# Optimization experiments

Measured on AMD Instinct MI355X. Metric: run time of the kernel, lower is better.

The kernel has to match this reference:

```python
import jax, jax.numpy as jnp
import numpy as np


def setup_inputs() -> dict:
    key = jax.random.key(0)
    kq, kk, kwq, kwk, kwv = jax.random.split(key, 5)
    B, T, C, H = 16, 2048, 1024, 64
    q = jax.random.normal(kq, (B, T, C), dtype=jnp.float32)
    k = jax.random.normal(kk, (B, T, C), dtype=jnp.float32)
    s = 1.0 / np.sqrt(C)
    Wq = jax.random.normal(kwq, (C, H), dtype=jnp.float32) * s
    Wk = jax.random.normal(kwk, (C, H), dtype=jnp.float32) * s
    Wv = jax.random.normal(kwv, (C, H), dtype=jnp.float32) * s
    return {"q": q, "k": k, "Wq": Wq, "Wk": Wk, "Wv": Wv}


def reference(q, k, Wq, Wk, Wv):
    # q, k: (B, T, C); projections are bias-free C -> head_size H
    Q = q @ Wq            # (B, T, H)
    K = k @ Wk            # (B, T, H)
    V = k @ Wv            # (B, T, H)
    T = q.shape[1]
    # NOTE: original scales by input dim C (q.shape[-1]), not head_size
    scale = q.shape[-1] ** (-0.5)
    wei = jnp.einsum('bth,bsh->bts', Q, K) * scale   # (B, T, T)
    causal = jnp.tril(jnp.ones((T, T), dtype=bool))
    wei = jnp.where(causal, wei, -jnp.inf)
    wei = jax.nn.softmax(wei, axis=-1)
    # dropout rate is 0.0 -> identity at inference
    out = jnp.einsum('bts,bsh->bth', wei, V)         # (B, T, H)
    return out
```

## Files before the change

kernel.cpp:

```cpp
#include <hip/hip_runtime.h>
#include <hip/hip_bf16.h>

typedef __bf16 bf16;
typedef __bf16 bf16x4 __attribute__((ext_vector_type(4)));
typedef __bf16 bf16x8 __attribute__((ext_vector_type(8)));
typedef float f32x4 __attribute__((ext_vector_type(4)));

#define MFMA_16x16x32(A, B, C) __builtin_amdgcn_mfma_f32_16x16x32_bf16(A, B, C, 0, 0, 0)

static_assert(sizeof(bf16x8) == 16, "bf16x8 must be 16B");

__global__ __launch_bounds__(256) void wtrans_kernel(
    const float* __restrict__ Wq, const float* __restrict__ Wk,
    const float* __restrict__ Wv, bf16* __restrict__ Wt)
{
  int idx = blockIdx.x * 256 + threadIdx.x;
  int p = idx >> 16;
  int rem = idx & 65535;
  int h = rem >> 10;
  int c = rem & 1023;
  const float* W = (p == 0) ? Wq : (p == 1) ? Wk : Wv;
  Wt[idx] = (bf16)W[c * 64 + h];
}

__global__ __launch_bounds__(1024, 4) void proj_kernel(
    const float* __restrict__ qin, const float* __restrict__ kin,
    const bf16* __restrict__ Wt,
    bf16* __restrict__ Qb, bf16* __restrict__ Kb, bf16* __restrict__ Vtb)
{
  extern __shared__ __align__(16) bf16 lds[];
  const int tid = threadIdx.x;
  const int lane = tid & 63;
  const int w = tid >> 6;
  const int g = lane >> 4;
  const int r = lane & 15;
  const int rl = lane >> 2;
  const int l4 = lane & 3;

  bf16* const stageW = lds + 65536 + w * 640;

  const int bid = blockIdx.x;
  const bool isQ = (bid < 128);
  const int fbid = isQ ? bid : bid - 128;
  const int strip = fbid * 16 + w;
  const float* A = isQ ? qin : kin;
  const float* ap = A + (size_t)strip * 16 * 1024;

  f32x4 acc0[4], acc1[4];
  #pragma unroll
  for (int cf = 0; cf < 4; cf++) {
    acc0[cf] = (f32x4){0.f, 0.f, 0.f, 0.f};
    acc1[cf] = (f32x4){0.f, 0.f, 0.f, 0.f};
  }

  auto afrag = [&](int c) -> bf16x8 {
    const float* rowp = ap + (size_t)rl * 1024 + c * 32 + l4 * 4;
    float4 a0 = *(const float4*)(rowp);
    float4 a1 = *(const float4*)(rowp + 16);
    bf16x4 w0 = (bf16x4){(bf16)a0.x, (bf16)a0.y, (bf16)a0.z, (bf16)a0.w};
    bf16x4 w1 = (bf16x4){(bf16)a1.x, (bf16)a1.y, (bf16)a1.z, (bf16)a1.w};
    *(bf16x4*)&stageW[rl * 40 + l4 * 4] = w0;
    *(bf16x4*)&stageW[rl * 40 + 16 + l4 * 4] = w1;
    return *(const bf16x8*)&stageW[r * 40 + g * 8];
  };

  if (isQ) {
    #pragma unroll
    for (int i = 0; i < 8; ++i) {
      int cid = i * 1024 + tid;
      int row = cid >> 7, ch = cid & 127;
      int pch = ch ^ (row & 7);
      *(bf16x8*)&lds[row * 1024 + pch * 8] =
          *(const bf16x8*)(Wt + (size_t)row * 1024 + ch * 8);
    }
    __syncthreads();

    #pragma unroll 2
    for (int c = 0; c < 32; ++c) {
      bf16x8 af = afrag(c);
      #pragma unroll
      for (int cf = 0; cf < 4; cf++) {
        int rw = cf * 16 + r;
        int pch = (4 * c + g) ^ (rw & 7);
        bf16x8 bfr = *(const bf16x8*)&lds[rw * 1024 + pch * 8];
        acc0[cf] = MFMA_16x16x32(af, bfr, acc0[cf]);
      }
    }

    #pragma unroll
    for (int cf = 0; cf < 4; cf++)
      #pragma unroll
      for (int jj = 0; jj < 4; jj++) {
        int rg = strip * 16 + g * 4 + jj;
        Qb[(size_t)rg * 64 + cf * 16 + r] = (bf16)acc0[cf][jj];
      }
  } else {
    for (int p = 0; p < 4; ++p) {
      __syncthreads();
      #pragma unroll
      for (int i = 0; i < 2; ++i) {
        int cid = i * 1024 + tid;
        int row = cid >> 5, ch = cid & 31;
        int pch = ch ^ (row & 7);
        *(bf16x8*)&lds[row * 256 + pch * 8] =
            *(const bf16x8*)(Wt + 65536 + (size_t)row * 1024 + p * 256 + ch * 8);
        *(bf16x8*)&lds[16384 + row * 256 + pch * 8] =
            *(const bf16x8*)(Wt + 2 * 65536 + (size_t)row * 1024 + p * 256 + ch * 8);
      }
      __syncthreads();

      #pragma unroll 2
      for (int cl = 0; cl < 8; ++cl) {
        bf16x8 af = afrag(p * 8 + cl);
        #pragma unroll
        for (int cf = 0; cf < 4; cf++) {
          int rw = cf * 16 + r;
          int pch = (4 * cl + g) ^ (rw & 7);
          bf16x8 b0 = *(const bf16x8*)&lds[rw * 256 + pch * 8];
          acc0[cf] = MFMA_16x16x32(af, b0, acc0[cf]);
          bf16x8 b1 = *(const bf16x8*)&lds[16384 + rw * 256 + pch * 8];
          acc1[cf] = MFMA_16x16x32(af, b1, acc1[cf]);
        }
      }
    }

    #pragma unroll
    for (int cf = 0; cf < 4; cf++)
      #pragma unroll
      for (int jj = 0; jj < 4; jj++) {
        int rg = strip * 16 + g * 4 + jj;
        Kb[(size_t)rg * 64 + cf * 16 + r] = (bf16)acc0[cf][jj];
      }
    int bb = (strip * 16) >> 11;
    int t0 = (strip * 16 + g * 4) & 2047;
    #pragma unroll
    for (int cf = 0; cf < 4; cf++) {
      bf16x4 v = (bf16x4){(bf16)acc1[cf][0], (bf16)acc1[cf][1],
                          (bf16)acc1[cf][2], (bf16)acc1[cf][3]};
      *(bf16x4*)&Vtb[((size_t)(bb * 64 + cf * 16 + r)) * 2048 + t0] = v;
    }
  }
}

__global__ __launch_bounds__(256) void attn_kernel(
    const bf16* __restrict__ Qb, const bf16* __restrict__ Kb,
    const bf16* __restrict__ Vtb, float* __restrict__ out)
{
  const int qt = (int)(gridDim.x - 1 - blockIdx.x);
  const int b = blockIdx.y;
  const int tid = threadIdx.x;
  const int lane = tid & 63;
  const int w = tid >> 6;
  const int g = lane >> 4;
  const int r = lane & 15;

  __shared__ __align__(16) bf16 Ks[64][80];
  __shared__ __align__(16) bf16 Vs[64][80];
  __shared__ __align__(16) bf16 Ps[4][16][80];

  const int q0 = qt * 64 + w * 16;
  const bf16* qp = Qb + (size_t)(b * 2048 + q0 + r) * 64 + g * 8;
  const bf16x8 qf0 = *(const bf16x8*)qp;
  const bf16x8 qf1 = *(const bf16x8*)(qp + 32);

  f32x4 acc_o[4];
  #pragma unroll
  for (int hf = 0; hf < 4; hf++) acc_o[hf] = (f32x4){0.f, 0.f, 0.f, 0.f};
  float m_r[4] = {-1e30f, -1e30f, -1e30f, -1e30f};
  float l_r[4] = {0.f, 0.f, 0.f, 0.f};
  const float scale = 0.03125f;

  const int sh = tid >> 2;
  const int sc = (tid & 3) * 16;

  for (int kv = 0; kv <= qt; kv++) {
    {
      const bf16* kp = Kb + (size_t)(b * 2048 + kv * 64 + sh) * 64 + sc;
      *(bf16x8*)&Ks[sh][sc]     = *(const bf16x8*)kp;
      *(bf16x8*)&Ks[sh][sc + 8] = *(const bf16x8*)(kp + 8);
      const bf16* vp = Vtb + (size_t)(b * 64 + sh) * 2048 + kv * 64 + sc;
      *(bf16x8*)&Vs[sh][sc]     = *(const bf16x8*)vp;
      *(bf16x8*)&Vs[sh][sc + 8] = *(const bf16x8*)(vp + 8);
    }
    __syncthreads();

    f32x4 s[4];
    #pragma unroll
    for (int cf = 0; cf < 4; cf++) {
      bf16x8 kf0 = *(const bf16x8*)&Ks[cf * 16 + r][g * 8];
      bf16x8 kf1 = *(const bf16x8*)&Ks[cf * 16 + r][32 + g * 8];
      f32x4 t = (f32x4){0.f, 0.f, 0.f, 0.f};
      t = MFMA_16x16x32(qf0, kf0, t);
      t = MFMA_16x16x32(qf1, kf1, t);
      s[cf] = t;
    }

    const bool diag = (kv == qt);
    float pm[4] = {-1e30f, -1e30f, -1e30f, -1e30f};
    #pragma unroll
    for (int cf = 0; cf < 4; cf++) {
      #pragma unroll
      for (int j = 0; j < 4; j++) {
        float v = s[cf][j] * scale;
        if (diag && (cf * 16 + r) > (w * 16 + g * 4 + j)) v = -1e30f;
        s[cf][j] = v;
        pm[j] = fmaxf(pm[j], v);
      }
    }
    #pragma unroll
    for (int j = 0; j < 4; j++) {
      #pragma unroll
      for (int msk = 1; msk < 16; msk <<= 1)
        pm[j] = fmaxf(pm[j], __shfl_xor(pm[j], msk, 64));
    }
    float corr[4];
    #pragma unroll
    for (int j = 0; j < 4; j++) {
      float mn = fmaxf(m_r[j], pm[j]);
      corr[j] = __expf(m_r[j] - mn);
      m_r[j] = mn;
    }
    float rs[4] = {0.f, 0.f, 0.f, 0.f};
    #pragma unroll
    for (int cf = 0; cf < 4; cf++) {
      #pragma unroll
      for (int j = 0; j < 4; j++) {
        float pv = __expf(s[cf][j] - m_r[j]);
        s[cf][j] = pv;
        rs[j] += pv;
      }
    }
    #pragma unroll
    for (int j = 0; j < 4; j++) {
      #pragma unroll
      for (int msk = 1; msk < 16; msk <<= 1)
        rs[j] += __shfl_xor(rs[j], msk, 64);
      l_r[j] = l_r[j] * corr[j] + rs[j];
    }
    #pragma unroll
    for (int hf = 0; hf < 4; hf++)
      #pragma unroll
      for (int j = 0; j < 4; j++)
        acc_o[hf][j] *= corr[j];

    #pragma unroll
    for (int cf = 0; cf < 4; cf++)
      #pragma unroll
      for (int j = 0; j < 4; j++)
        Ps[w][g * 4 + j][cf * 16 + r] = (bf16)s[cf][j];

    __syncthreads();

    #pragma unroll
    for (int ss = 0; ss < 2; ss++) {
      bf16x8 pf = *(const bf16x8*)&Ps[w][r][ss * 32 + g * 8];
      #pragma unroll
      for (int hf = 0; hf < 4; hf++) {
        bf16x8 vf = *(const bf16x8*)&Vs[hf * 16 + r][ss * 32 + g * 8];
        acc_o[hf] = MFMA_16x16x32(pf, vf, acc_o[hf]);
      }
    }
    __syncthreads();
  }

  float inv[4];
  #pragma unroll
  for (int j = 0; j < 4; j++) inv[j] = 1.0f / l_r[j];
  const size_t ob = (size_t)(b * 2048 + q0) * 64;
  #pragma unroll
  for (int hf = 0; hf < 4; hf++)
    #pragma unroll
    for (int j = 0; j < 4; j++)
      out[ob + (size_t)(g * 4 + j) * 64 + hf * 16 + r] = acc_o[hf][j] * inv[j];
}

extern "C" void kernel_launch(void* const* d_in, const int* in_sizes, int n_in,
                              void* d_out, int out_size, void* d_ws, size_t ws_size,
                              hipStream_t stream)
{
  const float* q  = (const float*)d_in[0];
  const float* k  = (const float*)d_in[1];
  const float* Wq = (const float*)d_in[2];
  const float* Wk = (const float*)d_in[3];
  const float* Wv = (const float*)d_in[4];
  float* out = (float*)d_out;

  char* ws = (char*)d_ws;
  bf16* Qb  = (bf16*)(ws);
  bf16* Kb  = (bf16*)(ws + (4u << 20));
  bf16* Vtb = (bf16*)(ws + (8u << 20));
  bf16* Wt  = (bf16*)(ws + (12u << 20));

  hipLaunchKernelGGL(wtrans_kernel, dim3(768), dim3(256), 0, stream,
                     Wq, Wk, Wv, Wt);
  hipLaunchKernelGGL(proj_kernel, dim3(256), dim3(1024), 151552, stream,
                     q, k, Wt, Qb, Kb, Vtb);
  hipLaunchKernelGGL(attn_kernel, dim3(32, 16), dim3(256), 0, stream,
                     Qb, Kb, Vtb, out);
}
```

Baseline: 125.9 us.

## Restructure projection kernel with batched A-loads, padded LDS, and smaller blocks

The projection kernel now runs 512 blocks of 512 threads (8 waves) instead of 256 blocks of 1024. Each wave loads a full 16x256 slab of activations with 16 coalesced float4 loads per lane before converting to bf16 into a padded LDS tile, replacing the per-MFMA gather-and-stage path. The Q and K/V paths share one four-phase loop over K with padded (stride-280) weight tiles instead of XOR swizzling. A __syncthreads between the P write and the PV MFMA in attention is also removed, relying on each wave only reading its own Ps slice, though other waves' Vs reads may still be constrained.

```diff
diff --git a/kernel.cpp b/kernel.cpp
--- a/kernel.cpp
+++ b/kernel.cpp
@@ -23,7 +23,7 @@
   Wt[idx] = (bf16)W[c * 64 + h];
 }
 
-__global__ __launch_bounds__(1024, 4) void proj_kernel(
+__global__ __launch_bounds__(512, 2) void proj_kernel(
     const float* __restrict__ qin, const float* __restrict__ kin,
     const bf16* __restrict__ Wt,
     bf16* __restrict__ Qb, bf16* __restrict__ Kb, bf16* __restrict__ Vtb)
@@ -34,17 +34,16 @@
   const int w = tid >> 6;
   const int g = lane >> 4;
   const int r = lane & 15;
-  const int rl = lane >> 2;
-  const int l4 = lane & 3;
-
-  bf16* const stageW = lds + 65536 + w * 640;
 
   const int bid = blockIdx.x;
-  const bool isQ = (bid < 128);
-  const int fbid = isQ ? bid : bid - 128;
-  const int strip = fbid * 16 + w;
+  const bool isQ = (bid < 256);
+  const int strip = (isQ ? bid : bid - 256) * 8 + w;
   const float* A = isQ ? qin : kin;
-  const float* ap = A + (size_t)strip * 16 * 1024;
+  const float* ap = A + (size_t)strip * 16 * 1024 + lane * 4;
+
+  bf16* const B0 = lds;
+  bf16* const B1 = lds + 17920;
+  bf16* const sA = lds + 35840 + w * 4480;
 
   f32x4 acc0[4], acc1[4];
   #pragma unroll
@@ -53,40 +52,52 @@
     acc1[cf] = (f32x4){0.f, 0.f, 0.f, 0.f};
   }
 
-  auto afrag = [&](int c) -> bf16x8 {
-    const float* rowp = ap + (size_t)rl * 1024 + c * 32 + l4 * 4;
-    float4 a0 = *(const float4*)(rowp);
-    float4 a1 = *(const float4*)(rowp + 16);
-    bf16x4 w0 = (bf16x4){(bf16)a0.x, (bf16)a0.y, (bf16)a0.z, (bf16)a0.w};
-    bf16x4 w1 = (bf16x4){(bf16)a1.x, (bf16)a1.y, (bf16)a1.z, (bf16)a1.w};
-    *(bf16x4*)&stageW[rl * 40 + l4 * 4] = w0;
-    *(bf16x4*)&stageW[rl * 40 + 16 + l4 * 4] = w1;
-    return *(const bf16x8*)&stageW[r * 40 + g * 8];
-  };
+  for (int q = 0; q < 4; ++q) {
+    if (q) __syncthreads();
+
+    #pragma unroll
+    for (int i = 0; i < 4; ++i) {
+      int c = i * 512 + tid;
+      int row = c >> 5, ch = c & 31;
+      bf16x8 v0 = *(const bf16x8*)(Wt + (size_t)(isQ ? 0 : 65536)
+                                   + (size_t)row * 1024 + q * 256 + ch * 8);
+      *(bf16x8*)&B0[row * 280 + ch * 8] = v0;
+      if (!isQ) {
+        bf16x8 v1 = *(const bf16x8*)(Wt + (size_t)2 * 65536
+                                     + (size_t)row * 1024 + q * 256 + ch * 8);
+        *(bf16x8*)&B1[row * 280 + ch * 8] = v1;
+      }
+    }
+    __syncthreads();
+
+    float4 L[16];
+    #pragma unroll
+    for (int i = 0; i < 16; ++i)
+      L[i] = *(const float4*)(ap + (size_t)i * 1024 + q * 256);
+
+    #pragma unroll
+    for (int i = 0; i < 16; ++i) {
+      bf16x4 v = (bf16x4){(bf16)L[i].x, (bf16)L[i].y,
+                          (bf16)L[i].z, (bf16)L[i].w};
+      *(bf16x4*)&sA[i * 280 + lane * 4] = v;
+    }
+
+    #pragma unroll
+    for (int cl = 0; cl < 8; ++cl) {
+      bf16x8 af = *(const bf16x8*)&sA[r * 280 + cl * 32 + g * 8];
+      #pragma unroll
+      for (int cf = 0; cf < 4; cf++) {
+        bf16x8 b0 = *(const bf16x8*)&B0[(cf * 16 + r) * 280 + cl * 32 + g * 8];
+        acc0[cf] = MFMA_16x16x32(af, b0, acc0[cf]);
+        if (!isQ) {
+          bf16x8 b1 = *(const bf16x8*)&B1[(cf * 16 + r) * 280 + cl * 32 + g * 8];
+          acc1[cf] = MFMA_16x16x32(af, b1, acc1[cf]);
+        }
+      }
+    }
+  }
 
   if (isQ) {
-    #pragma unroll
-    for (int i = 0; i < 8; ++i) {
-      int cid = i * 1024 + tid;
-      int row = cid >> 7, ch = cid & 127;
-      int pch = ch ^ (row & 7);
-      *(bf16x8*)&lds[row * 1024 + pch * 8] =
-          *(const bf16x8*)(Wt + (size_t)row * 1024 + ch * 8);
-    }
-    __syncthreads();
-
-    #pragma unroll 2
-    for (int c = 0; c < 32; ++c) {
-      bf16x8 af = afrag(c);
-      #pragma unroll
-      for (int cf = 0; cf < 4; cf++) {
-        int rw = cf * 16 + r;
-        int pch = (4 * c + g) ^ (rw & 7);
-        bf16x8 bfr = *(const bf16x8*)&lds[rw * 1024 + pch * 8];
-        acc0[cf] = MFMA_16x16x32(af, bfr, acc0[cf]);
-      }
-    }
-
     #pragma unroll
     for (int cf = 0; cf < 4; cf++)
       #pragma unroll
@@ -95,35 +106,6 @@
         Qb[(size_t)rg * 64 + cf * 16 + r] = (bf16)acc0[cf][jj];
       }
   } else {
-    for (int p = 0; p < 4; ++p) {
-      __syncthreads();
-      #pragma unroll
-      for (int i = 0; i < 2; ++i) {
-        int cid = i * 1024 + tid;
-        int row = cid >> 5, ch = cid & 31;
-        int pch = ch ^ (row & 7);
-        *(bf16x8*)&lds[row * 256 + pch * 8] =
-            *(const bf16x8*)(Wt + 65536 + (size_t)row * 1024 + p * 256 + ch * 8);
-        *(bf16x8*)&lds[16384 + row * 256 + pch * 8] =
-            *(const bf16x8*)(Wt + 2 * 65536 + (size_t)row * 1024 + p * 256 + ch * 8);
-      }
-      __syncthreads();
-
-      #pragma unroll 2
-      for (int cl = 0; cl < 8; ++cl) {
-        bf16x8 af = afrag(p * 8 + cl);
-        #pragma unroll
-        for (int cf = 0; cf < 4; cf++) {
-          int rw = cf * 16 + r;
-          int pch = (4 * cl + g) ^ (rw & 7);
-          bf16x8 b0 = *(const bf16x8*)&lds[rw * 256 + pch * 8];
-          acc0[cf] = MFMA_16x16x32(af, b0, acc0[cf]);
-          bf16x8 b1 = *(const bf16x8*)&lds[16384 + rw * 256 + pch * 8];
-          acc1[cf] = MFMA_16x16x32(af, b1, acc1[cf]);
-        }
-      }
-    }
-
     #pragma unroll
     for (int cf = 0; cf < 4; cf++)
       #pragma unroll
@@ -249,8 +231,6 @@
       for (int j = 0; j < 4; j++)
         Ps[w][g * 4 + j][cf * 16 + r] = (bf16)s[cf][j];
 
-    __syncthreads();
-
     #pragma unroll
     for (int ss = 0; ss < 2; ss++) {
       bf16x8 pf = *(const bf16x8*)&Ps[w][r][ss * 32 + g * 8];
@@ -293,7 +273,7 @@
 
   hipLaunchKernelGGL(wtrans_kernel, dim3(768), dim3(256), 0, stream,
                      Wq, Wk, Wv, Wt);
-  hipLaunchKernelGGL(proj_kernel, dim3(256), dim3(1024), 151552, stream,
+  hipLaunchKernelGGL(proj_kernel, dim3(512), dim3(512), 143360, stream,
                      q, k, Wt, Qb, Kb, Vtb);
   hipLaunchKernelGGL(attn_kernel, dim3(32, 16), dim3(256), 0, stream,
                      Qb, Kb, Vtb, out);
```

Measured after the change: 152.1 us. 1.21x slower.
